# Kernel tuning notes

Measured on AMD Instinct MI355X. Metric: run time of the kernel, lower is better.

Reference implementation:

```python
import jax, jax.numpy as jnp
import numpy as np

B, T, V, C, H, E, O, NL = 2048, 128, 256, 32, 128, 256, 256, 3
BN = E // 8  # bottleneck = 32
G = 3 * H    # stacked gate dim (r,z,n) = 384
LN_EPS = 1e-5


def setup_inputs() -> dict:
    key = jax.random.key(0)
    ks = jax.random.split(key, 19)
    s = 0.1
    return {
        "tokens": jax.random.randint(ks[0], (B, T), 0, V),
        "lang_ids": jax.random.randint(ks[1], (B,), 0, NL),
        "char_embed": jax.random.normal(ks[2], (V, C)) * s,
        "w_ih_f": jax.random.normal(ks[3], (G, C)) * s,
        "w_hh_f": jax.random.normal(ks[4], (G, H)) * s,
        "b_ih_f": jax.random.normal(ks[5], (G,)) * s,
        "b_hh_f": jax.random.normal(ks[6], (G,)) * s,
        "w_ih_b": jax.random.normal(ks[7], (G, C)) * s,
        "w_hh_b": jax.random.normal(ks[8], (G, H)) * s,
        "b_ih_b": jax.random.normal(ks[9], (G,)) * s,
        "b_hh_b": jax.random.normal(ks[10], (G,)) * s,
        "down_w": jax.random.normal(ks[11], (NL, BN, E)) * s,
        "down_b": jax.random.normal(ks[12], (NL, BN)) * s,
        "up_w": jax.random.normal(ks[13], (NL, E, BN)) * s,
        "up_b": jax.random.normal(ks[14], (NL, E)) * s,
        "ln_g": jnp.ones((NL, E)),
        "ln_b": jnp.zeros((NL, E)),
        "proj_w": jax.random.normal(ks[15], (O, E)) * s,
        "proj_b": jax.random.normal(ks[16], (O,)) * s,
    }


def _gru_last_hidden(x, w_ih, w_hh, b_ih, b_hh):
    """x: [B,T,C] -> final hidden [B,H]. torch GRU gate order (r,z,n)."""
    xp = jnp.einsum('btc,gc->btg', x, w_ih) + b_ih        # [B,T,3H]
    xp = jnp.swapaxes(xp, 0, 1)                           # [T,B,3H]
    h0 = jnp.zeros((x.shape[0], w_hh.shape[1]), x.dtype)

    def step(h, xp_t):
        gh = h @ w_hh.T + b_hh
        xr, xz, xn = jnp.split(xp_t, 3, axis=-1)
        hr, hz, hn = jnp.split(gh, 3, axis=-1)
        r = jax.nn.sigmoid(xr + hr)
        z = jax.nn.sigmoid(xz + hz)
        n = jnp.tanh(xn + r * hn)
        return (1.0 - z) * n + z * h, None

    hT, _ = jax.lax.scan(step, h0, xp)
    return hT


def reference(tokens, lang_ids, char_embed,
              w_ih_f, w_hh_f, b_ih_f, b_hh_f,
              w_ih_b, w_hh_b, b_ih_b, b_hh_b,
              down_w, down_b, up_w, up_b, ln_g, ln_b,
              proj_w, proj_b):
    emb = char_embed[tokens]                              # [B,T,C]
    h_f = _gru_last_hidden(emb, w_ih_f, w_hh_f, b_ih_f, b_hh_f)
    h_b = _gru_last_hidden(emb[:, ::-1], w_ih_b, w_hh_b, b_ih_b, b_hh_b)
    feat = jnp.concatenate([h_f, h_b], axis=-1)           # [B,E]

    # per-sample language-routed bottleneck adapter (gathered expert params)
    hid = jax.nn.gelu(
        jnp.einsum('be,bde->bd', feat, down_w[lang_ids]) + down_b[lang_ids],
        approximate=False)                                # [B,BN]
    adapted = jnp.einsum('bd,bed->be', hid, up_w[lang_ids]) + up_b[lang_ids]
    x = feat + adapted
    mu = jnp.mean(x, axis=-1, keepdims=True)
    var = jnp.var(x, axis=-1, keepdims=True)
    xn = (x - mu) / jnp.sqrt(var + LN_EPS)
    y = xn * ln_g[lang_ids] + ln_b[lang_ids]              # [B,E]

    return y @ proj_w.T + proj_b                          # [B,O]
```

## Files before the change

kernel.cpp:

```cpp
#include <hip/hip_runtime.h>
#include <hip/hip_bf16.h>
#include <hip/hip_fp16.h>

#define Bn 2048
#define Tn 128
#define Vn 256
#define Cn 32
#define Hn 128
#define En 256
#define On 256
#define Gn 384
#define BNn 32

typedef _Float16 f16;
typedef __attribute__((ext_vector_type(8))) _Float16 h8;
typedef __attribute__((ext_vector_type(4))) _Float16 h4;
typedef __attribute__((ext_vector_type(4))) float f4;

#define LOG2E 1.4426950408889634f

__device__ __forceinline__ float fexp2(float x) { return __builtin_amdgcn_exp2f(x); }
__device__ __forceinline__ float frcp(float x) { return __builtin_amdgcn_rcpf(x); }

__global__ void build_table_k(const float* __restrict__ emb,
                              const float* __restrict__ wf,
                              const float* __restrict__ bfv,
                              const float* __restrict__ wb,
                              const float* __restrict__ bbv,
                              f16* __restrict__ xt) {
  const int dir = blockIdx.x >> 8;
  const int v = blockIdx.x & 255;
  const int j = threadIdx.x;
  const float* w = dir ? wb : wf;
  const float* bi = dir ? bbv : bfv;
  const float sc[3] = {-LOG2E, -LOG2E, 2.0f * LOG2E};
  h4 o;
  o[3] = (f16)0.f;
#pragma unroll
  for (int ga = 0; ga < 3; ++ga) {
    const int g = ga * Hn + j;
    float acc = bi[g];
    const f4* wr = (const f4*)(w + g * Cn);
    const f4* er = (const f4*)(emb + v * Cn);
#pragma unroll
    for (int q = 0; q < 8; ++q) {
      f4 wv = wr[q], ev = er[q];
      acc = fmaf(ev.x, wv.x, acc);
      acc = fmaf(ev.y, wv.y, acc);
      acc = fmaf(ev.z, wv.z, acc);
      acc = fmaf(ev.w, wv.w, acc);
    }
    o[ga] = (f16)(acc * sc[ga]);
  }
  *(h4*)&xt[((dir * Vn + v) * Hn + j) * 4] = o;
}

__launch_bounds__(512, 2)
__global__ void gru_k(const int* __restrict__ tokens,
                      const float* __restrict__ whhf,
                      const float* __restrict__ bhhf,
                      const float* __restrict__ whhb,
                      const float* __restrict__ bhhb,
                      const f16* __restrict__ xt,
                      float* __restrict__ feat) {
  const int dir = blockIdx.x & 1;
  const int b0 = (blockIdx.x >> 1) * 16;
  const int tid = threadIdx.x;
  const int wv = tid >> 6;
  const int ln = tid & 63;
  const int lr = ln & 15;
  const int lg = ln >> 4;
  const int j0 = wv * 16;
  const int j = j0 + lr;

  __shared__ f16 hfrag[2 * 2048];
  __shared__ f16 xstg[2 * 8192];
  __shared__ int tokl[16 * 128];

  for (int i = tid; i < 16 * 128; i += 512)
    tokl[i] = tokens[(b0 + (i >> 7)) * Tn + (i & 127)];
  for (int i = tid; i < 2 * 2048; i += 512) hfrag[i] = (f16)0.f;

  const float* whh = dir ? whhb : whhf;
  const float* bhh = dir ? bhhb : bhhf;
  const f16* tab = xt + dir * (Vn * Hn * 4);

  const float gsc[3] = {-LOG2E, -LOG2E, 2.0f * LOG2E};
  h8 Bf[3][4];
#pragma unroll
  for (int ga = 0; ga < 3; ++ga) {
    const float* wr = whh + (ga * Hn + j) * Hn + lg * 8;
#pragma unroll
    for (int kk = 0; kk < 4; ++kk) {
      h8 b;
#pragma unroll
      for (int i = 0; i < 8; ++i) b[i] = (f16)(wr[kk * 32 + i] * gsc[ga]);
      Bf[ga][kk] = b;
    }
  }
  const float bh0 = bhh[j] * (-LOG2E);
  const float bh1 = bhh[Hn + j] * (-LOG2E);
  const float bh2 = bhh[2 * Hn + j] * (2.0f * LOG2E);

  const int ss = tid >> 5;
  const int sq = tid & 31;

  {
    const int tt = dir ? (Tn - 1) : 0;
    const int tok = tokl[ss * 128 + tt];
    const h8* src = (const h8*)(tab + tok * 512 + sq * 16);
    h8 v0 = src[0], v1 = src[1];
    *(h8*)&xstg[ss * 512 + sq * 16] = v0;
    *(h8*)&xstg[ss * 512 + sq * 16 + 8] = v1;
  }
  __syncthreads();

  const int aoff = lg * 256 + lr * 16;
  const int woff = (j >> 3) * 256 + (j & 7) * 2 + lg * 64;
  const int xoff = lg * 4096 + j * 8;

  float hprev[4] = {0.f, 0.f, 0.f, 0.f};
  int p = 0;

  for (int t = 0; t < Tn; ++t) {
    const int cur = t & 1, nxt = cur ^ 1;
    const int tn = (t + 1 < Tn) ? (t + 1) : t;
    const int tt2 = dir ? (Tn - 1 - tn) : tn;
    const int tok2 = tokl[ss * 128 + tt2];
    const h8* src = (const h8*)(tab + tok2 * 512 + sq * 16);
    h8 v0 = src[0], v1 = src[1];

    const char* hb = (const char*)hfrag + p * 4096;
    h8 Af[4];
#pragma unroll
    for (int kk = 0; kk < 4; ++kk)
      Af[kk] = *(const h8*)(hb + kk * 1024 + aoff);

    f4 aR = {bh0, bh0, bh0, bh0};
    f4 aZ = {bh1, bh1, bh1, bh1};
    f4 aN = {bh2, bh2, bh2, bh2};
#pragma unroll
    for (int kk = 0; kk < 4; ++kk) {
      aR = __builtin_amdgcn_mfma_f32_16x16x32_f16(Af[kk], Bf[0][kk], aR, 0, 0, 0);
      aZ = __builtin_amdgcn_mfma_f32_16x16x32_f16(Af[kk], Bf[1][kk], aZ, 0, 0, 0);
      aN = __builtin_amdgcn_mfma_f32_16x16x32_f16(Af[kk], Bf[2][kk], aN, 0, 0, 0);
    }

    const char* xb = (const char*)xstg + cur * 16384;
    char* hw = (char*)hfrag + (p ^ 1) * 4096;
#pragma unroll
    for (int r = 0; r < 4; ++r) {
      h4 xv = *(const h4*)(xb + xoff + r * 1024);
      const float sr = (float)xv[0], sz = (float)xv[1], sn = (float)xv[2];
      const float rg = frcp(1.0f + fexp2(sr + aR[r]));
      const float zg = frcp(1.0f + fexp2(sz + aZ[r]));
      const float ng = fmaf(-2.0f, frcp(1.0f + fexp2(fmaf(rg, aN[r], sn))), 1.0f);
      const float hn_ = fmaf(zg, hprev[r] - ng, ng);
      hprev[r] = hn_;
      *(f16*)(hw + woff + r * 16) = (f16)hn_;
    }

    *(h8*)((char*)xstg + nxt * 16384 + ss * 1024 + sq * 32) = v0;
    *(h8*)((char*)xstg + nxt * 16384 + ss * 1024 + sq * 32 + 16) = v1;

    __syncthreads();
    p ^= 1;
  }

#pragma unroll
  for (int r = 0; r < 4; ++r)
    feat[(b0 + lg * 4 + r) * En + dir * Hn + j] = hprev[r];
}

__launch_bounds__(256, 2)
__global__ void epi_k(const float* __restrict__ feat,
                      const int* __restrict__ lang_ids,
                      const float* __restrict__ down_w,
                      const float* __restrict__ down_b,
                      const float* __restrict__ up_w,
                      const float* __restrict__ up_b,
                      const float* __restrict__ ln_g,
                      const float* __restrict__ ln_b,
                      const float* __restrict__ proj_w,
                      const float* __restrict__ proj_b,
                      float* __restrict__ out) {
  const int tid = threadIdx.x;
  const int wv = tid >> 6, ln = tid & 63;
  const int b0 = blockIdx.x * 8;

  __shared__ float fl[8][En];
  __shared__ f16 yA[16][En + 8];

#pragma unroll
  for (int s = 0; s < 8; ++s) fl[s][tid] = feat[(b0 + s) * En + tid];
  {
    f16* z = &yA[0][0];
    for (int i = tid; i < 16 * (En + 8); i += 256) z[i] = (f16)0.f;
  }
  __syncthreads();

#pragma unroll 1
  for (int si = 0; si < 2; ++si) {
    const int s = wv * 2 + si;
    const int lang = lang_ids[b0 + s];

    const int d = ln & 31, hf = ln >> 5;
    const f4* dwv = (const f4*)(down_w + (lang * BNn + d) * En + hf * 128);
    const f4* fsv = (const f4*)&fl[s][hf * 128];
    float pacc = 0.f;
#pragma unroll
    for (int q = 0; q < 32; ++q) {
      f4 a = fsv[q], w = dwv[q];
      pacc = fmaf(a.x, w.x, pacc);
      pacc = fmaf(a.y, w.y, pacc);
      pacc = fmaf(a.z, w.z, pacc);
      pacc = fmaf(a.w, w.w, pacc);
    }
    pacc += __shfl_xor(pacc, 32);
    const float hv = pacc + down_b[lang * BNn + d];
    const float hid = 0.5f * hv * (1.0f + erff(hv * 0.70710678118f));

    float hh[32];
#pragma unroll
    for (int dd = 0; dd < 32; ++dd) hh[dd] = __shfl(hid, dd);

    const int e0 = ln * 4;
    float x[4];
    float s1 = 0.f, s2 = 0.f;
#pragma unroll
    for (int i = 0; i < 4; ++i) {
      const f4* ur = (const f4*)(up_w + (lang * En + e0 + i) * BNn);
      float a = 0.f;
#pragma unroll
      for (int q = 0; q < 8; ++q) {
        f4 u = ur[q];
        a = fmaf(hh[q * 4 + 0], u.x, a);
        a = fmaf(hh[q * 4 + 1], u.y, a);
        a = fmaf(hh[q * 4 + 2], u.z, a);
        a = fmaf(hh[q * 4 + 3], u.w, a);
      }
      x[i] = a + fl[s][e0 + i] + up_b[lang * En + e0 + i];
      s1 += x[i];
      s2 = fmaf(x[i], x[i], s2);
    }
#pragma unroll
    for (int off = 32; off >= 1; off >>= 1) {
      s1 += __shfl_xor(s1, off);
      s2 += __shfl_xor(s2, off);
    }
    const float mu = s1 * (1.0f / En);
    const float var = s2 * (1.0f / En) - mu * mu;
    const float rs = rsqrtf(var + 1e-5f);
#pragma unroll
    for (int i = 0; i < 4; ++i) {
      const float yv = (x[i] - mu) * rs * ln_g[lang * En + e0 + i] + ln_b[lang * En + e0 + i];
      yA[s][e0 + i] = (f16)yv;
    }
  }
  __syncthreads();

  const int lr = ln & 15, lg = ln >> 4;
  f4 acc[4];
#pragma unroll
  for (int tt = 0; tt < 4; ++tt) {
    const float pb = proj_b[wv * 64 + tt * 16 + lr];
    acc[tt] = (f4){pb, pb, pb, pb};
  }
#pragma unroll
  for (int kk = 0; kk < 8; ++kk) {
    h8 aF = *(const h8*)(&yA[lr][kk * 32 + lg * 8]);
#pragma unroll
    for (int tt = 0; tt < 4; ++tt) {
      const int o0 = wv * 64 + tt * 16;
      const float* pw = proj_w + (o0 + lr) * En + kk * 32 + lg * 8;
      h8 bF;
#pragma unroll
      for (int i = 0; i < 8; ++i) bF[i] = (f16)pw[i];
      acc[tt] = __builtin_amdgcn_mfma_f32_16x16x32_f16(aF, bF, acc[tt], 0, 0, 0);
    }
  }
  if (lg < 2) {
#pragma unroll
    for (int tt = 0; tt < 4; ++tt) {
      const int o0 = wv * 64 + tt * 16;
#pragma unroll
      for (int r = 0; r < 4; ++r)
        out[(b0 + lg * 4 + r) * On + o0 + lr] = acc[tt][r];
    }
  }
}

extern "C" void kernel_launch(void* const* d_in, const int* in_sizes, int n_in,
                              void* d_out, int out_size, void* d_ws, size_t ws_size,
                              hipStream_t stream) {
  const int* tokens = (const int*)d_in[0];
  const int* lang_ids = (const int*)d_in[1];
  const float* emb = (const float*)d_in[2];
  const float* w_ih_f = (const float*)d_in[3];
  const float* w_hh_f = (const float*)d_in[4];
  const float* b_ih_f = (const float*)d_in[5];
  const float* b_hh_f = (const float*)d_in[6];
  const float* w_ih_b = (const float*)d_in[7];
  const float* w_hh_b = (const float*)d_in[8];
  const float* b_ih_b = (const float*)d_in[9];
  const float* b_hh_b = (const float*)d_in[10];
  const float* down_w = (const float*)d_in[11];
  const float* down_b = (const float*)d_in[12];
  const float* up_w = (const float*)d_in[13];
  const float* up_b = (const float*)d_in[14];
  const float* ln_g = (const float*)d_in[15];
  const float* ln_b = (const float*)d_in[16];
  const float* proj_w = (const float*)d_in[17];
  const float* proj_b = (const float*)d_in[18];

  f16* xt = (f16*)d_ws;
  float* feat = (float*)((char*)d_ws + 2 * Vn * Hn * 4 * 2);

  build_table_k<<<dim3(512), dim3(128), 0, stream>>>(emb, w_ih_f, b_ih_f, w_ih_b, b_ih_b, xt);
  gru_k<<<dim3(256), dim3(512), 0, stream>>>(tokens, w_hh_f, b_hh_f, w_hh_b, b_hh_b, xt, feat);
  epi_k<<<dim3(256), dim3(256), 0, stream>>>(feat, lang_ids, down_w, down_b, up_w, up_b,
                                             ln_g, ln_b, proj_w, proj_b, (float*)d_out);
}
```

Before: 141.0 us.

## Shrink GRU blocks to 8 sequences with 4 waves each, prefetch x into registers

The GRU kernel now processes 8 sequences per block with 4 waves, each wave covering 32 hidden units (two 16-column MFMA tiles), and launches twice as many blocks. The LDS staging buffer for input projections is removed: each lane prefetches its next-step gate inputs straight from the table into registers. The goal is more blocks in flight, lower per-step sync cost with fewer waves, and no LDS round-trip for x. In exchange, half the MFMA rows (lanes with lg>=2) do wasted work on padding, and register pressure roughly doubles from the extra weight fragments.

```diff
diff --git a/kernel.cpp b/kernel.cpp
--- a/kernel.cpp
+++ b/kernel.cpp
@@ -55,7 +55,7 @@
   *(h4*)&xt[((dir * Vn + v) * Hn + j) * 4] = o;
 }
 
-__launch_bounds__(512, 2)
+__launch_bounds__(256, 2)
 __global__ void gru_k(const int* __restrict__ tokens,
                       const float* __restrict__ whhf,
                       const float* __restrict__ bhhf,
@@ -64,112 +64,137 @@
                       const f16* __restrict__ xt,
                       float* __restrict__ feat) {
   const int dir = blockIdx.x & 1;
-  const int b0 = (blockIdx.x >> 1) * 16;
+  const int b0 = (blockIdx.x >> 1) * 8;
   const int tid = threadIdx.x;
   const int wv = tid >> 6;
   const int ln = tid & 63;
   const int lr = ln & 15;
   const int lg = ln >> 4;
-  const int j0 = wv * 16;
-  const int j = j0 + lr;
+  const int j0 = wv * 32;
 
   __shared__ f16 hfrag[2 * 2048];
-  __shared__ f16 xstg[2 * 8192];
-  __shared__ int tokl[16 * 128];
-
-  for (int i = tid; i < 16 * 128; i += 512)
+  __shared__ int tokl[8 * 128];
+
+  for (int i = tid; i < 8 * 128; i += 256)
     tokl[i] = tokens[(b0 + (i >> 7)) * Tn + (i & 127)];
-  for (int i = tid; i < 2 * 2048; i += 512) hfrag[i] = (f16)0.f;
+  for (int i = tid; i < 2 * 2048; i += 256) hfrag[i] = (f16)0.f;
 
   const float* whh = dir ? whhb : whhf;
   const float* bhh = dir ? bhhb : bhhf;
   const f16* tab = xt + dir * (Vn * Hn * 4);
 
   const float gsc[3] = {-LOG2E, -LOG2E, 2.0f * LOG2E};
-  h8 Bf[3][4];
-#pragma unroll
-  for (int ga = 0; ga < 3; ++ga) {
-    const float* wr = whh + (ga * Hn + j) * Hn + lg * 8;
-#pragma unroll
-    for (int kk = 0; kk < 4; ++kk) {
-      h8 b;
-#pragma unroll
-      for (int i = 0; i < 8; ++i) b[i] = (f16)(wr[kk * 32 + i] * gsc[ga]);
-      Bf[ga][kk] = b;
-    }
-  }
-  const float bh0 = bhh[j] * (-LOG2E);
-  const float bh1 = bhh[Hn + j] * (-LOG2E);
-  const float bh2 = bhh[2 * Hn + j] * (2.0f * LOG2E);
-
-  const int ss = tid >> 5;
-  const int sq = tid & 31;
-
-  {
+  h8 Bf[2][3][4];
+  float bh[2][3];
+#pragma unroll
+  for (int jt = 0; jt < 2; ++jt) {
+    const int j = j0 + jt * 16 + lr;
+#pragma unroll
+    for (int ga = 0; ga < 3; ++ga) {
+      const float* wr = whh + (ga * Hn + j) * Hn + lg * 8;
+#pragma unroll
+      for (int kk = 0; kk < 4; ++kk) {
+        h8 b;
+#pragma unroll
+        for (int i = 0; i < 8; ++i) b[i] = (f16)(wr[kk * 32 + i] * gsc[ga]);
+        Bf[jt][ga][kk] = b;
+      }
+      bh[jt][ga] = bhh[ga * Hn + j] * gsc[ga];
+    }
+  }
+
+  __syncthreads();
+
+  const int aoff = lg * 256 + lr * 16;
+  int wo[2];
+#pragma unroll
+  for (int jt = 0; jt < 2; ++jt) {
+    const int j = j0 + jt * 16 + lr;
+    wo[jt] = (j >> 3) * 256 + (j & 7) * 2 + lg * 64;
+  }
+  const int sbase = (lg & 1) * 4;
+
+  h4 xc[8], xn[8];
+#pragma unroll
+  for (int i = 0; i < 8; ++i) xc[i] = (h4)0;
+
+  if (lg < 2) {
     const int tt = dir ? (Tn - 1) : 0;
-    const int tok = tokl[ss * 128 + tt];
-    const h8* src = (const h8*)(tab + tok * 512 + sq * 16);
-    h8 v0 = src[0], v1 = src[1];
-    *(h8*)&xstg[ss * 512 + sq * 16] = v0;
-    *(h8*)&xstg[ss * 512 + sq * 16 + 8] = v1;
-  }
-  __syncthreads();
-
-  const int aoff = lg * 256 + lr * 16;
-  const int woff = (j >> 3) * 256 + (j & 7) * 2 + lg * 64;
-  const int xoff = lg * 4096 + j * 8;
-
-  float hprev[4] = {0.f, 0.f, 0.f, 0.f};
+#pragma unroll
+    for (int r = 0; r < 4; ++r) {
+      const int tok = tokl[(sbase + r) * 128 + tt];
+      xc[r] = *(const h4*)(tab + tok * 512 + (j0 + lr) * 4);
+      xc[4 + r] = *(const h4*)(tab + tok * 512 + (j0 + 16 + lr) * 4);
+    }
+  }
+
+  float hprev[8] = {0.f, 0.f, 0.f, 0.f, 0.f, 0.f, 0.f, 0.f};
   int p = 0;
 
   for (int t = 0; t < Tn; ++t) {
-    const int cur = t & 1, nxt = cur ^ 1;
     const int tn = (t + 1 < Tn) ? (t + 1) : t;
     const int tt2 = dir ? (Tn - 1 - tn) : tn;
-    const int tok2 = tokl[ss * 128 + tt2];
-    const h8* src = (const h8*)(tab + tok2 * 512 + sq * 16);
-    h8 v0 = src[0], v1 = src[1];
+    if (lg < 2) {
+#pragma unroll
+      for (int r = 0; r < 4; ++r) {
+        const int tok = tokl[(sbase + r) * 128 + tt2];
+        xn[r] = *(const h4*)(tab + tok * 512 + (j0 + lr) * 4);
+        xn[4 + r] = *(const h4*)(tab + tok * 512 + (j0 + 16 + lr) * 4);
+      }
+    }
 
     const char* hb = (const char*)hfrag + p * 4096;
-    h8 Af[4];
-#pragma unroll
-    for (int kk = 0; kk < 4; ++kk)
-      Af[kk] = *(const h8*)(hb + kk * 1024 + aoff);
-
-    f4 aR = {bh0, bh0, bh0, bh0};
-    f4 aZ = {bh1, bh1, bh1, bh1};
-    f4 aN = {bh2, bh2, bh2, bh2};
+    f4 acc[2][3];
+#pragma unroll
+    for (int jt = 0; jt < 2; ++jt)
+#pragma unroll
+      for (int ga = 0; ga < 3; ++ga)
+        acc[jt][ga] = (f4){bh[jt][ga], bh[jt][ga], bh[jt][ga], bh[jt][ga]};
 #pragma unroll
     for (int kk = 0; kk < 4; ++kk) {
-      aR = __builtin_amdgcn_mfma_f32_16x16x32_f16(Af[kk], Bf[0][kk], aR, 0, 0, 0);
-      aZ = __builtin_amdgcn_mfma_f32_16x16x32_f16(Af[kk], Bf[1][kk], aZ, 0, 0, 0);
-      aN = __builtin_amdgcn_mfma_f32_16x16x32_f16(Af[kk], Bf[2][kk], aN, 0, 0, 0);
-    }
-
-    const char* xb = (const char*)xstg + cur * 16384;
+      h8 a = *(const h8*)(hb + kk * 1024 + aoff);
+#pragma unroll
+      for (int jt = 0; jt < 2; ++jt) {
+        acc[jt][0] = __builtin_amdgcn_mfma_f32_16x16x32_f16(a, Bf[jt][0][kk], acc[jt][0], 0, 0, 0);
+        acc[jt][1] = __builtin_amdgcn_mfma_f32_16x16x32_f16(a, Bf[jt][1][kk], acc[jt][1], 0, 0, 0);
+        acc[jt][2] = __builtin_amdgcn_mfma_f32_16x16x32_f16(a, Bf[jt][2][kk], acc[jt][2], 0, 0, 0);
+      }
+    }
+
+#pragma unroll
+    for (int jt = 0; jt < 2; ++jt)
+#pragma unroll
+      for (int r = 0; r < 4; ++r) {
+        const h4 xv = xc[jt * 4 + r];
+        const float rg = frcp(1.0f + fexp2((float)xv[0] + acc[jt][0][r]));
+        const float zg = frcp(1.0f + fexp2((float)xv[1] + acc[jt][1][r]));
+        const float ng = fmaf(-2.0f, frcp(1.0f + fexp2(fmaf(rg, acc[jt][2][r], (float)xv[2]))), 1.0f);
+        hprev[jt * 4 + r] = fmaf(zg, hprev[jt * 4 + r] - ng, ng);
+      }
+
     char* hw = (char*)hfrag + (p ^ 1) * 4096;
-#pragma unroll
-    for (int r = 0; r < 4; ++r) {
-      h4 xv = *(const h4*)(xb + xoff + r * 1024);
-      const float sr = (float)xv[0], sz = (float)xv[1], sn = (float)xv[2];
-      const float rg = frcp(1.0f + fexp2(sr + aR[r]));
-      const float zg = frcp(1.0f + fexp2(sz + aZ[r]));
-      const float ng = fmaf(-2.0f, frcp(1.0f + fexp2(fmaf(rg, aN[r], sn))), 1.0f);
-      const float hn_ = fmaf(zg, hprev[r] - ng, ng);
-      hprev[r] = hn_;
-      *(f16*)(hw + woff + r * 16) = (f16)hn_;
-    }
-
-    *(h8*)((char*)xstg + nxt * 16384 + ss * 1024 + sq * 32) = v0;
-    *(h8*)((char*)xstg + nxt * 16384 + ss * 1024 + sq * 32 + 16) = v1;
+    if (lg < 2) {
+#pragma unroll
+      for (int jt = 0; jt < 2; ++jt)
+#pragma unroll
+        for (int r = 0; r < 4; ++r)
+          *(f16*)(hw + wo[jt] + r * 16) = (f16)hprev[jt * 4 + r];
+    }
+
+#pragma unroll
+    for (int i = 0; i < 8; ++i) xc[i] = xn[i];
 
     __syncthreads();
     p ^= 1;
   }
 
-#pragma unroll
-  for (int r = 0; r < 4; ++r)
-    feat[(b0 + lg * 4 + r) * En + dir * Hn + j] = hprev[r];
+  if (lg < 2) {
+#pragma unroll
+    for (int jt = 0; jt < 2; ++jt)
+#pragma unroll
+      for (int r = 0; r < 4; ++r)
+        feat[(b0 + lg * 4 + r) * En + dir * Hn + (j0 + jt * 16 + lr)] = hprev[jt * 4 + r];
+  }
 }
 
 __launch_bounds__(256, 2)
@@ -317,7 +342,7 @@
   float* feat = (float*)((char*)d_ws + 2 * Vn * Hn * 4 * 2);
 
   build_table_k<<<dim3(512), dim3(128), 0, stream>>>(emb, w_ih_f, b_ih_f, w_ih_b, b_ih_b, xt);
-  gru_k<<<dim3(256), dim3(512), 0, stream>>>(tokens, w_hh_f, b_hh_f, w_hh_b, b_hh_b, xt, feat);
+  gru_k<<<dim3(512), dim3(256), 0, stream>>>(tokens, w_hh_f, b_hh_f, w_hh_b, b_hh_b, xt, feat);
   epi_k<<<dim3(256), dim3(256), 0, stream>>>(feat, lang_ids, down_w, down_b, up_w, up_b,
                                              ln_g, ln_b, proj_w, proj_b, (float*)d_out);
 }
```

Result: slower. 211.8 us (+50.2%).

## Prefetch GRU input projections into registers instead of LDS staging

Applied to the files above, without the earlier changes.

The GRU kernel no longer stages next-step input projections through a double-buffered shared-memory array. Each lane now loads the four h4 gate values it needs directly from the global table into registers one step ahead, and rotates them at the end of the step. The __syncthreads call is replaced by an inline lgkmcnt wait plus s_barrier, and the main loop is kept rolled. This removes the LDS write and read traffic and frees 32KB of shared memory per block, which may allow more blocks per CU. The cost is scattered 8-byte global loads per lane on the serial critical path, with latency that must be hidden within one step.

```diff
diff --git a/kernel.cpp b/kernel.cpp
--- a/kernel.cpp
+++ b/kernel.cpp
@@ -74,7 +74,6 @@
   const int j = j0 + lr;
 
   __shared__ f16 hfrag[2 * 2048];
-  __shared__ f16 xstg[2 * 8192];
   __shared__ int tokl[16 * 128];
 
   for (int i = tid; i < 16 * 128; i += 512)
@@ -102,68 +101,64 @@
   const float bh1 = bhh[Hn + j] * (-LOG2E);
   const float bh2 = bhh[2 * Hn + j] * (2.0f * LOG2E);
 
-  const int ss = tid >> 5;
-  const int sq = tid & 31;
-
+  __syncthreads();
+
+  const int aoff = lg * 256 + lr * 16;
+  const int woff = (j >> 3) * 256 + (j & 7) * 2 + lg * 64;
+
+  h4 xc[4], xn[4];
   {
     const int tt = dir ? (Tn - 1) : 0;
-    const int tok = tokl[ss * 128 + tt];
-    const h8* src = (const h8*)(tab + tok * 512 + sq * 16);
-    h8 v0 = src[0], v1 = src[1];
-    *(h8*)&xstg[ss * 512 + sq * 16] = v0;
-    *(h8*)&xstg[ss * 512 + sq * 16 + 8] = v1;
-  }
-  __syncthreads();
-
-  const int aoff = lg * 256 + lr * 16;
-  const int woff = (j >> 3) * 256 + (j & 7) * 2 + lg * 64;
-  const int xoff = lg * 4096 + j * 8;
+#pragma unroll
+    for (int r = 0; r < 4; ++r) {
+      const int tok = tokl[(lg * 4 + r) * 128 + tt];
+      xc[r] = *(const h4*)(tab + tok * 512 + j * 4);
+    }
+  }
 
   float hprev[4] = {0.f, 0.f, 0.f, 0.f};
   int p = 0;
 
+#pragma unroll 1
   for (int t = 0; t < Tn; ++t) {
-    const int cur = t & 1, nxt = cur ^ 1;
     const int tn = (t + 1 < Tn) ? (t + 1) : t;
     const int tt2 = dir ? (Tn - 1 - tn) : tn;
-    const int tok2 = tokl[ss * 128 + tt2];
-    const h8* src = (const h8*)(tab + tok2 * 512 + sq * 16);
-    h8 v0 = src[0], v1 = src[1];
+#pragma unroll
+    for (int r = 0; r < 4; ++r) {
+      const int tok = tokl[(lg * 4 + r) * 128 + tt2];
+      xn[r] = *(const h4*)(tab + tok * 512 + j * 4);
+    }
 
     const char* hb = (const char*)hfrag + p * 4096;
-    h8 Af[4];
-#pragma unroll
-    for (int kk = 0; kk < 4; ++kk)
-      Af[kk] = *(const h8*)(hb + kk * 1024 + aoff);
-
     f4 aR = {bh0, bh0, bh0, bh0};
     f4 aZ = {bh1, bh1, bh1, bh1};
     f4 aN = {bh2, bh2, bh2, bh2};
 #pragma unroll
     for (int kk = 0; kk < 4; ++kk) {
-      aR = __builtin_amdgcn_mfma_f32_16x16x32_f16(Af[kk], Bf[0][kk], aR, 0, 0, 0);
-      aZ = __builtin_amdgcn_mfma_f32_16x16x32_f16(Af[kk], Bf[1][kk], aZ, 0, 0, 0);
-      aN = __builtin_amdgcn_mfma_f32_16x16x32_f16(Af[kk], Bf[2][kk], aN, 0, 0, 0);
-    }
-
-    const char* xb = (const char*)xstg + cur * 16384;
+      h8 a = *(const h8*)(hb + kk * 1024 + aoff);
+      aR = __builtin_amdgcn_mfma_f32_16x16x32_f16(a, Bf[0][kk], aR, 0, 0, 0);
+      aZ = __builtin_amdgcn_mfma_f32_16x16x32_f16(a, Bf[1][kk], aZ, 0, 0, 0);
+      aN = __builtin_amdgcn_mfma_f32_16x16x32_f16(a, Bf[2][kk], aN, 0, 0, 0);
+    }
+
+#pragma unroll
+    for (int r = 0; r < 4; ++r) {
+      const h4 xv = xc[r];
+      const float rg = frcp(1.0f + fexp2((float)xv[0] + aR[r]));
+      const float zg = frcp(1.0f + fexp2((float)xv[1] + aZ[r]));
+      const float ng = fmaf(-2.0f, frcp(1.0f + fexp2(fmaf(rg, aN[r], (float)xv[2]))), 1.0f);
+      hprev[r] = fmaf(zg, hprev[r] - ng, ng);
+    }
+
     char* hw = (char*)hfrag + (p ^ 1) * 4096;
 #pragma unroll
-    for (int r = 0; r < 4; ++r) {
-      h4 xv = *(const h4*)(xb + xoff + r * 1024);
-      const float sr = (float)xv[0], sz = (float)xv[1], sn = (float)xv[2];
-      const float rg = frcp(1.0f + fexp2(sr + aR[r]));
-      const float zg = frcp(1.0f + fexp2(sz + aZ[r]));
-      const float ng = fmaf(-2.0f, frcp(1.0f + fexp2(fmaf(rg, aN[r], sn))), 1.0f);
-      const float hn_ = fmaf(zg, hprev[r] - ng, ng);
-      hprev[r] = hn_;
-      *(f16*)(hw + woff + r * 16) = (f16)hn_;
-    }
-
-    *(h8*)((char*)xstg + nxt * 16384 + ss * 1024 + sq * 32) = v0;
-    *(h8*)((char*)xstg + nxt * 16384 + ss * 1024 + sq * 32 + 16) = v1;
-
-    __syncthreads();
+    for (int r = 0; r < 4; ++r)
+      *(f16*)(hw + woff + r * 16) = (f16)hprev[r];
+
+#pragma unroll
+    for (int r = 0; r < 4; ++r) xc[r] = xn[r];
+
+    asm volatile("s_waitcnt lgkmcnt(0)\n\ts_barrier" ::: "memory");
     p ^= 1;
   }
 
```

New measurement: 131.1 us. -7.0%, faster.
